# Performance work log

Hardware: AMD Instinct MI355X
Metric: run time of the kernel (lower is better)

The kernel has to match this reference:

```python
import jax, jax.numpy as jnp
import numpy as np
import math

EMBED = 768
HEADS = 12
DK = EMBED // HEADS
FFN = 3072
NQ = 8
B, S = 4, 2048


def _layernorm(x, g, b, eps=1e-5):
    mu = jnp.mean(x, axis=-1, keepdims=True)
    var = jnp.var(x, axis=-1, keepdims=True)
    return (x - mu) * jax.lax.rsqrt(var + eps) * g + b


def setup_inputs() -> dict:
    key = jax.random.key(0)
    ks = jax.random.split(key, 16)
    std = 0.02
    inp = {
        "x": jax.random.normal(ks[0], (B, S, EMBED), dtype=jnp.float32),
        "mask": jnp.ones((B, S), dtype=jnp.int32),
        # attention projections (torch Linear: W [out, in])
        "wq": jax.random.normal(ks[1], (EMBED, EMBED), jnp.float32) * std,
        "bq": jnp.zeros((EMBED,), jnp.float32),
        "wk": jax.random.normal(ks[2], (EMBED, EMBED), jnp.float32) * std,
        "bk": jnp.zeros((EMBED,), jnp.float32),
        "wv": jax.random.normal(ks[3], (EMBED, EMBED), jnp.float32) * std,
        "bv": jnp.zeros((EMBED,), jnp.float32),
        "wo": jax.random.normal(ks[4], (EMBED, EMBED), jnp.float32) * std,
        "bo": jnp.zeros((EMBED,), jnp.float32),
        # layernorms
        "g1": jnp.ones((EMBED,), jnp.float32),
        "be1": jnp.zeros((EMBED,), jnp.float32),
        "g2": jnp.ones((EMBED,), jnp.float32),
        "be2": jnp.zeros((EMBED,), jnp.float32),
        # quantum FFN: trainable RY angles + two linears
        "theta": jax.random.normal(ks[5], (NQ,), jnp.float32) * 0.1,
        "w1": jax.random.normal(ks[6], (FFN, NQ), jnp.float32) * std,
        "b1": jnp.zeros((FFN,), jnp.float32),
        "w2": jax.random.normal(ks[7], (EMBED, FFN), jnp.float32) * std,
        "b2": jnp.zeros((EMBED,), jnp.float32),
    }
    return inp


def _block(x, mask, wq, bq, wk, bk, wv, bv, wo, bo, g1, be1, g2, be2,
           theta, w1, b1, w2, b2):
    b, s, _ = x.shape
    # --- multi-head attention (dropout = identity at eval) ---
    q = (x @ wq.T + bq).reshape(b, s, HEADS, DK)
    k = (x @ wk.T + bk).reshape(b, s, HEADS, DK)
    v = (x @ wv.T + bv).reshape(b, s, HEADS, DK)
    scores = jnp.einsum("bqhd,bkhd->bhqk", q, k) / math.sqrt(DK)
    scores = jnp.where(mask[:, None, None, :] == 0, -1e9, scores)
    attn = jax.nn.softmax(scores, axis=-1)
    ctx = jnp.einsum("bhqk,bkhd->bqhd", attn, v).reshape(b, s, EMBED)
    attn_out = ctx @ wo.T + bo
    x = _layernorm(x + attn_out, g1, be1)
    # --- quantum FFN: RY(x_i) then RY(theta_i) on |0>, <Z> = cos(x_i+theta_i)
    # (product state, no entanglement -> exact closed form, fully batched)
    meas = jnp.cos(x[..., :NQ] + theta)            # [b, s, NQ]
    h = jax.nn.relu(meas @ w1.T + b1)              # [b, s, FFN]
    ffn_out = h @ w2.T + b2                        # [b, s, EMBED]
    return _layernorm(x + ffn_out, g2, be2)


def reference(x, mask, wq, bq, wk, bk, wv, bv, wo, bo, g1, be1, g2, be2,
              theta, w1, b1, w2, b2):
    return _block(x, mask, wq, bq, wk, bk, wv, bv, wo, bo,
                  g1, be1, g2, be2, theta, w1, b1, w2, b2)
```

## Files before the change

### kernel.cpp

```cpp
#include <hip/hip_runtime.h>
#include <hip/hip_bf16.h>


typedef __bf16 bf16_t;
typedef bf16_t bf16x4 __attribute__((ext_vector_type(4)));
typedef bf16_t bf16x8 __attribute__((ext_vector_type(8)));
typedef float floatx4 __attribute__((ext_vector_type(4)));

#define LOG2E 1.44269504088896f

__device__ __forceinline__ void gload16(const bf16_t* g, bf16_t* l) {
    __builtin_amdgcn_global_load_lds(
        (const __attribute__((address_space(1))) unsigned int*)g,
        (__attribute__((address_space(3))) unsigned int*)l,
        16, 0, 0);
}

__global__ __launch_bounds__(256)
void prep(const float* __restrict__ x,
          const float* __restrict__ wq, const float* __restrict__ wk,
          const float* __restrict__ wv, const float* __restrict__ wo,
          const float* __restrict__ w2, const float* __restrict__ w1,
          const float* __restrict__ bq, const float* __restrict__ bk,
          const float* __restrict__ bv,
          bf16_t* __restrict__ xb, bf16_t* __restrict__ wqkv,
          bf16_t* __restrict__ wob, bf16_t* __restrict__ w2b,
          bf16_t* __restrict__ w1b, float* __restrict__ bqkv)
{
    const int seg = blockIdx.y;
    const int idx = blockIdx.x * 256 + threadIdx.x;
    if (seg == 0) {
        if (idx >= 1572864) return;
        const float4 f = ((const float4*)x)[idx];
        bf16x4 o = {(bf16_t)f.x, (bf16_t)f.y, (bf16_t)f.z, (bf16_t)f.w};
        ((bf16x4*)xb)[idx] = o;
    } else if (seg == 1) {
        if (idx >= 442368) return;
        const int e = idx * 4;
        float4 f = (e < 589824) ? ((const float4*)wq)[idx]
                 : (e < 1179648) ? ((const float4*)wk)[idx - 147456]
                                 : ((const float4*)wv)[idx - 294912];
        if (e < 589824) { f.x *= 0.125f; f.y *= 0.125f; f.z *= 0.125f; f.w *= 0.125f; }
        bf16x4 o = {(bf16_t)f.x, (bf16_t)f.y, (bf16_t)f.z, (bf16_t)f.w};
        ((bf16x4*)wqkv)[idx] = o;
    } else if (seg == 2) {
        if (idx >= 147456) return;
        const float4 f = ((const float4*)wo)[idx];
        bf16x4 o = {(bf16_t)f.x, (bf16_t)f.y, (bf16_t)f.z, (bf16_t)f.w};
        ((bf16x4*)wob)[idx] = o;
    } else if (seg == 3) {
        if (idx >= 589824) return;
        const float4 f = ((const float4*)w2)[idx];
        bf16x4 o = {(bf16_t)f.x, (bf16_t)f.y, (bf16_t)f.z, (bf16_t)f.w};
        ((bf16x4*)w2b)[idx] = o;
    } else if (seg == 4) {
        if (idx >= 576) return;
        const int e = idx * 4;
        float4 f = (e < 768) ? ((const float4*)bq)[idx]
                 : (e < 1536) ? ((const float4*)bk)[idx - 192]
                              : ((const float4*)bv)[idx - 384];
        if (e < 768) { f.x *= 0.125f; f.y *= 0.125f; f.z *= 0.125f; f.w *= 0.125f; }
        ((float4*)bqkv)[idx] = f;
    } else {
        if (idx >= 6144) return;
        const float4 f = ((const float4*)w1)[idx];
        bf16x4 o = {(bf16_t)f.x, (bf16_t)f.y, (bf16_t)f.z, (bf16_t)f.w};
        ((bf16x4*)w1b)[idx] = o;
    }
}

template<typename TC>
__global__ __launch_bounds__(256)
void gemm_bb(const bf16_t* __restrict__ A, const bf16_t* __restrict__ W,
             const float* __restrict__ bias, TC* __restrict__ C,
             int kPer, int lda, int ldw, int ldc, int splitStride)
{
    __shared__ __align__(16) bf16_t As[2][4096];
    __shared__ __align__(16) bf16_t Bs[2][4096];
    const int tid  = threadIdx.x;
    const int wave = tid >> 6;
    const int lane = tid & 63;
    const int wm = (wave >> 1) * 64;
    const int wn = (wave & 1) * 64;

    const int nwg  = gridDim.x * gridDim.y;
    const int flat = blockIdx.y * gridDim.x + blockIdx.x;
    const int swzb = (flat & 7) * (nwg >> 3) + (flat >> 3);
    const int bm = (swzb / gridDim.x) * 128;
    const int bn = (swzb % gridDim.x) * 128;

    const int fr = lane & 15;
    const int fk = (lane >> 4) * 8;

    const int kBeg = blockIdx.z * kPer;
    const int kEnd = kBeg + kPer;
    C += (size_t)blockIdx.z * splitStride;

    const int srow = tid >> 2;
    const int scol = (tid & 3) * 8;

    floatx4 acc[4][4] = {};

    const bf16_t* gA = A + (size_t)(bm + srow) * lda + scol;
    const bf16_t* gB = W + (size_t)(bn + srow) * ldw + scol;

#define STAGE(buf, kk)                                              \
    {   const bf16_t* ga = gA + (kk);                               \
        const bf16_t* gb = gB + (kk);                               \
        gload16(ga,                    &As[buf][tid * 8]);          \
        gload16(ga + (size_t)64 * lda, &As[buf][tid * 8 + 2048]);   \
        gload16(gb,                    &Bs[buf][tid * 8]);          \
        gload16(gb + (size_t)64 * ldw, &Bs[buf][tid * 8 + 2048]);   \
    }

    STAGE(0, kBeg);
    __syncthreads();

    int cur = 0;
    for (int k0 = kBeg; k0 < kEnd; k0 += 32) {
        if (k0 + 32 < kEnd) STAGE(cur ^ 1, k0 + 32);

        bf16x8 fa[4], fb[4];
        #pragma unroll
        for (int i = 0; i < 4; ++i) {
            fa[i] = *(const bf16x8*)&As[cur][(wm + i * 16 + fr) * 32 + fk];
            fb[i] = *(const bf16x8*)&Bs[cur][(wn + i * 16 + fr) * 32 + fk];
        }
        #pragma unroll
        for (int mi = 0; mi < 4; ++mi)
            #pragma unroll
            for (int ni = 0; ni < 4; ++ni)
                acc[mi][ni] = __builtin_amdgcn_mfma_f32_16x16x32_bf16(
                    fa[mi], fb[ni], acc[mi][ni], 0, 0, 0);

        __syncthreads();
        cur ^= 1;
    }
#undef STAGE

    const int fg = (lane >> 4) * 4;
    const bool addb = (blockIdx.z == 0);
    #pragma unroll
    for (int mi = 0; mi < 4; ++mi) {
        #pragma unroll
        for (int ni = 0; ni < 4; ++ni) {
            const int col = bn + wn + ni * 16 + fr;
            const float bv = addb ? bias[col] : 0.f;
            #pragma unroll
            for (int r = 0; r < 4; ++r) {
                const int row = bm + wm + mi * 16 + fg + r;
                C[(size_t)row * ldc + col] = (TC)(acc[mi][ni][r] + bv);
            }
        }
    }
}

__global__ __launch_bounds__(256)
void attn_mfma(const bf16_t* __restrict__ qkv, const int* __restrict__ mask,
               bf16_t* __restrict__ ctx)
{
    __shared__ bf16_t Ks[64][72];
    __shared__ bf16_t Vt[80][72];
    __shared__ float  mb_s[64];
    __shared__ bf16_t Pl[4][32][72];

    const int flat = blockIdx.x;
    const int swzb = (flat & 7) * 96 + (flat >> 3);
    const int bh = swzb >> 4;
    const int b = bh / 12, h = bh % 12;
    const int tid  = threadIdx.x;
    const int wave = tid >> 6;
    const int lane = tid & 63;
    const int g    = lane >> 4;
    const int fr   = lane & 15;
    const int qbase = (swzb & 15) * 128 + wave * 32;

    for (int idx = tid; idx < 16 * 72; idx += 256) {
        const int rr = idx / 72, cc = idx % 72;
        Vt[64 + rr][cc] = (bf16_t)(rr == 0 ? 1.f : 0.f);
    }

    bf16x8 qf[2][2];
    #pragma unroll
    for (int qt = 0; qt < 2; ++qt)
        #pragma unroll
        for (int s = 0; s < 2; ++s) {
            const size_t tok = (size_t)(b * 2048 + qbase + qt * 16 + fr);
            qf[qt][s] = *(const bf16x8*)(qkv + tok * 2304 + h * 64 + s * 32 + g * 8);
        }

    floatx4 o[2][4] = {};
    floatx4 oe[2] = {};

    const int skey = tid & 63;
    const int sgrp = tid >> 6;

    bf16x8 rk0, rk1, rv0, rv1;
    float  rmb;
    {
        const size_t ktok = (size_t)(b * 2048 + skey) * 2304 + h * 64;
        rk0 = *(const bf16x8*)(qkv + ktok + 768 + sgrp * 16);
        rk1 = *(const bf16x8*)(qkv + ktok + 768 + sgrp * 16 + 8);
        rv0 = *(const bf16x8*)(qkv + ktok + 1536 + sgrp * 16);
        rv1 = *(const bf16x8*)(qkv + ktok + 1536 + sgrp * 16 + 8);
        rmb = (mask[b * 2048 + skey] == 0) ? -1e9f : 0.f;
    }

    for (int kt = 0; kt < 32; ++kt) {
        __syncthreads();
        *(bf16x8*)&Ks[skey][sgrp * 16]     = rk0;
        *(bf16x8*)&Ks[skey][sgrp * 16 + 8] = rk1;
        #pragma unroll
        for (int j = 0; j < 8; ++j) {
            Vt[sgrp * 16 + j][skey]     = rv0[j];
            Vt[sgrp * 16 + 8 + j][skey] = rv1[j];
        }
        if (tid < 64) mb_s[tid] = rmb;
        __syncthreads();

        if (kt + 1 < 32) {
            const size_t ktok = (size_t)(b * 2048 + (kt + 1) * 64 + skey) * 2304 + h * 64;
            rk0 = *(const bf16x8*)(qkv + ktok + 768 + sgrp * 16);
            rk1 = *(const bf16x8*)(qkv + ktok + 768 + sgrp * 16 + 8);
            rv0 = *(const bf16x8*)(qkv + ktok + 1536 + sgrp * 16);
            rv1 = *(const bf16x8*)(qkv + ktok + 1536 + sgrp * 16 + 8);
            rmb = (mask[b * 2048 + (kt + 1) * 64 + skey] == 0) ? -1e9f : 0.f;
        }

        floatx4 st_[2][4] = {};
        #pragma unroll
        for (int s = 0; s < 2; ++s) {
            bf16x8 kf[4];
            #pragma unroll
            for (int ct = 0; ct < 4; ++ct)
                kf[ct] = *(const bf16x8*)&Ks[ct * 16 + fr][s * 32 + g * 8];
            #pragma unroll
            for (int qt = 0; qt < 2; ++qt)
                #pragma unroll
                for (int ct = 0; ct < 4; ++ct)
                    st_[qt][ct] = __builtin_amdgcn_mfma_f32_16x16x32_bf16(
                        kf[ct], qf[qt][s], st_[qt][ct], 0, 0, 0);
        }

        #pragma unroll
        for (int qt = 0; qt < 2; ++qt) {
            #pragma unroll
            for (int ct = 0; ct < 4; ++ct) {
                const float4 mb4 = *(const float4*)&mb_s[ct * 16 + g * 4];
                const float mbr[4] = { mb4.x, mb4.y, mb4.z, mb4.w };
                bf16x4 pw;
                #pragma unroll
                for (int r = 0; r < 4; ++r)
                    pw[r] = (bf16_t)__builtin_amdgcn_exp2f(
                        fmaf(st_[qt][ct][r], LOG2E, mbr[r]));
                *(bf16x4*)&Pl[wave][qt * 16 + fr][ct * 16 + g * 4] = pw;
            }
        }

        #pragma unroll
        for (int st2 = 0; st2 < 2; ++st2) {
            bf16x8 pf[2];
            #pragma unroll
            for (int qt = 0; qt < 2; ++qt)
                pf[qt] = *(const bf16x8*)&Pl[wave][qt * 16 + fr][st2 * 32 + g * 8];
            #pragma unroll
            for (int dt = 0; dt < 4; ++dt) {
                const bf16x8 vf = *(const bf16x8*)&Vt[dt * 16 + fr][st2 * 32 + g * 8];
                #pragma unroll
                for (int qt = 0; qt < 2; ++qt)
                    o[qt][dt] = __builtin_amdgcn_mfma_f32_16x16x32_bf16(
                        pf[qt], vf, o[qt][dt], 0, 0, 0);
            }
            const bf16x8 vo = *(const bf16x8*)&Vt[64 + fr][st2 * 32 + g * 8];
            #pragma unroll
            for (int qt = 0; qt < 2; ++qt)
                oe[qt] = __builtin_amdgcn_mfma_f32_16x16x32_bf16(
                    pf[qt], vo, oe[qt], 0, 0, 0);
        }
    }

    #pragma unroll
    for (int qt = 0; qt < 2; ++qt) {
        float inv[4];
        #pragma unroll
        for (int r = 0; r < 4; ++r) {
            const float lv = __shfl(oe[qt][r], (lane & 48), 64);
            inv[r] = 1.f / lv;
        }
        #pragma unroll
        for (int dt = 0; dt < 4; ++dt)
            #pragma unroll
            for (int r = 0; r < 4; ++r) {
                const size_t row = (size_t)(b * 2048 + qbase + qt * 16 + g * 4 + r);
                ctx[row * 768 + h * 64 + dt * 16 + fr] = (bf16_t)(o[qt][dt][r] * inv[r]);
            }
    }
}

__global__ __launch_bounds__(256)
void ln_fuse(const float* __restrict__ xin, const float* __restrict__ proj,
             const float* __restrict__ proj2,
             const float* __restrict__ g, const float* __restrict__ be,
             float* __restrict__ out,
             const float* __restrict__ theta, float* __restrict__ meas)
{
    const int wave = threadIdx.x >> 6;
    const int lane = threadIdx.x & 63;
    const int row  = blockIdx.x * 4 + wave;
    const size_t base = (size_t)row * 768;

    float4 v[3];
    float s1 = 0.f, s2 = 0.f;
    #pragma unroll
    for (int i = 0; i < 3; ++i) {
        const int c4 = lane + i * 64;
        const float4 a  = ((const float4*)(xin  + base))[c4];
        const float4 p  = ((const float4*)(proj + base))[c4];
        const float4 p2 = ((const float4*)(proj2 + base))[c4];
        v[i].x = a.x + p.x + p2.x;
        v[i].y = a.y + p.y + p2.y;
        v[i].z = a.z + p.z + p2.z;
        v[i].w = a.w + p.w + p2.w;
        s1 += v[i].x + v[i].y + v[i].z + v[i].w;
        s2 += v[i].x*v[i].x + v[i].y*v[i].y + v[i].z*v[i].z + v[i].w*v[i].w;
    }
    #pragma unroll
    for (int mk = 32; mk >= 1; mk >>= 1) {
        s1 += __shfl_xor(s1, mk, 64);
        s2 += __shfl_xor(s2, mk, 64);
    }
    const float mu   = s1 * (1.f / 768.f);
    const float var  = s2 * (1.f / 768.f) - mu * mu;
    const float rinv = rsqrtf(var + 1e-5f);

    #pragma unroll
    for (int i = 0; i < 3; ++i) {
        const int c4 = lane + i * 64;
        const float4 gg = ((const float4*)g)[c4];
        const float4 bb = ((const float4*)be)[c4];
        float4 o;
        o.x = (v[i].x - mu) * rinv * gg.x + bb.x;
        o.y = (v[i].y - mu) * rinv * gg.y + bb.y;
        o.z = (v[i].z - mu) * rinv * gg.z + bb.z;
        o.w = (v[i].w - mu) * rinv * gg.w + bb.w;
        ((float4*)(out + base))[c4] = o;
        if (i == 0 && meas != nullptr && lane < 2) {
            meas[row * 8 + lane * 4 + 0] = cosf(o.x + theta[lane * 4 + 0]);
            meas[row * 8 + lane * 4 + 1] = cosf(o.y + theta[lane * 4 + 1]);
            meas[row * 8 + lane * 4 + 2] = cosf(o.z + theta[lane * 4 + 2]);
            meas[row * 8 + lane * 4 + 3] = cosf(o.w + theta[lane * 4 + 3]);
        }
    }
}

__global__ __launch_bounds__(256)
void ffn1(const float* __restrict__ meas, const bf16_t* __restrict__ w1b,
          const float* __restrict__ b1, bf16_t* __restrict__ h)
{
    const int row0 = blockIdx.x * 4;
    __shared__ float ms[4][8];
    if (threadIdx.x < 32)
        ms[threadIdx.x >> 3][threadIdx.x & 7] = meas[row0 * 8 + threadIdx.x];
    __syncthreads();
    #pragma unroll
    for (int i = 0; i < 12; ++i) {
        const int f = threadIdx.x + i * 256;
        const bf16x8 w = *(const bf16x8*)(w1b + f * 8);
        float wv[8];
        #pragma unroll
        for (int j = 0; j < 8; ++j) wv[j] = (float)w[j];
        const float bias = b1[f];
        #pragma unroll
        for (int r = 0; r < 4; ++r) {
            float v = bias;
            #pragma unroll
            for (int j = 0; j < 8; ++j) v += ms[r][j] * wv[j];
            h[(size_t)(row0 + r) * 3072 + f] = (bf16_t)fmaxf(v, 0.f);
        }
    }
}

extern "C" void kernel_launch(void* const* d_in, const int* in_sizes, int n_in,
                              void* d_out, int out_size, void* d_ws, size_t ws_size,
                              hipStream_t stream)
{
    const float* x     = (const float*)d_in[0];
    const int*   mask  = (const int*)d_in[1];
    const float* wq    = (const float*)d_in[2];
    const float* bq    = (const float*)d_in[3];
    const float* wk    = (const float*)d_in[4];
    const float* bk    = (const float*)d_in[5];
    const float* wv    = (const float*)d_in[6];
    const float* bv    = (const float*)d_in[7];
    const float* wo    = (const float*)d_in[8];
    const float* bo    = (const float*)d_in[9];
    const float* g1    = (const float*)d_in[10];
    const float* be1   = (const float*)d_in[11];
    const float* g2    = (const float*)d_in[12];
    const float* be2   = (const float*)d_in[13];
    const float* theta = (const float*)d_in[14];
    const float* w1    = (const float*)d_in[15];
    const float* b1    = (const float*)d_in[16];
    const float* w2    = (const float*)d_in[17];
    const float* b2    = (const float*)d_in[18];
    float* out = (float*)d_out;

    char* ws = (char*)d_ws;
    bf16_t* qkv    = (bf16_t*)(ws + 0);
    bf16_t* ctx    = (bf16_t*)(ws + 37748736);
    float*  attnp  = (float*)(ws + 50331648);
    float*  y      = (float*)(ws + 100663296);
    float*  meas   = (float*)(ws + 125829120);
    bf16_t* xb     = (bf16_t*)(ws + 126091264);
    bf16_t* wqkv   = (bf16_t*)(ws + 138674176);
    bf16_t* wob    = (bf16_t*)(ws + 142213120);
    bf16_t* w2b    = (bf16_t*)(ws + 143392768);
    float*  bqkv   = (float*)(ws + 148111360);
    bf16_t* w1b    = (bf16_t*)(ws + 148120576);
    float*  ffnp   = (float*)(ws + 0);
    bf16_t* h      = (bf16_t*)(ws + 50331648);

    const dim3 blk(256);

    prep<<<dim3(6144, 6), blk, 0, stream>>>(x, wq, wk, wv, wo, w2, w1, bq, bk, bv,
                                            xb, wqkv, wob, w2b, w1b, bqkv);

    gemm_bb<bf16_t><<<dim3(18, 64, 1), blk, 0, stream>>>(
        xb, wqkv, bqkv, qkv, 768, 768, 768, 2304, 0);

    attn_mfma<<<dim3(768), blk, 0, stream>>>(qkv, mask, ctx);

    gemm_bb<float><<<dim3(6, 64, 2), blk, 0, stream>>>(
        ctx, wob, bo, attnp, 384, 768, 768, 768, 6291456);

    ln_fuse<<<dim3(2048), blk, 0, stream>>>(x, attnp, attnp + 6291456,
                                            g1, be1, y, theta, meas);

    ffn1<<<dim3(2048), blk, 0, stream>>>(meas, w1b, b1, h);

    gemm_bb<float><<<dim3(6, 64, 2), blk, 0, stream>>>(
        h, w2b, b2, ffnp, 1536, 3072, 3072, 768, 6291456);

    ln_fuse<<<dim3(2048), blk, 0, stream>>>(y, ffnp, ffnp + 6291456,
                                            g2, be2, out, nullptr, nullptr);
}
```

Measured before the change: 279.1 us.

## Emit head-major swizzled K/V from QKV GEMM and stream K via direct LDS loads

Adds a dedicated QKV GEMM whose epilogue writes Q token-major and K and V in a per-(batch, head) contiguous layout, with K columns XOR-swizzled by row. The attention kernel then streams each 64-key K tile straight into double-buffered LDS with global_load_lds, and loads V as contiguous 16-byte chunks instead of strided per-token reads. The aim is to remove register staging and bank conflicts for K and to make K/V fetches coalesced. In exchange the GEMM epilogue does scattered 2-byte stores into the head-major layout, and LDS use grows because K is now double-buffered.

```diff
diff --git a/kernel.cpp b/kernel.cpp
--- a/kernel.cpp
+++ b/kernel.cpp
@@ -156,10 +156,107 @@
 }
 
 __global__ __launch_bounds__(256)
-void attn_mfma(const bf16_t* __restrict__ qkv, const int* __restrict__ mask,
+void gemm_qkv(const bf16_t* __restrict__ A, const bf16_t* __restrict__ W0,
+              const float* __restrict__ bias0,
+              bf16_t* __restrict__ Qb, bf16_t* __restrict__ Kh,
+              bf16_t* __restrict__ Vh)
+{
+    __shared__ __align__(16) bf16_t As[2][4096];
+    __shared__ __align__(16) bf16_t Bs[2][4096];
+    const int tid  = threadIdx.x;
+    const int wave = tid >> 6;
+    const int lane = tid & 63;
+    const int wm = (wave >> 1) * 64;
+    const int wn = (wave & 1) * 64;
+
+    const int nwg  = gridDim.x * gridDim.y;
+    const int flat = blockIdx.y * gridDim.x + blockIdx.x;
+    const int swzb = (flat & 7) * (nwg >> 3) + (flat >> 3);
+    const int tx = swzb % gridDim.x;
+    const int bm = (swzb / gridDim.x) * 128;
+    const int sect = tx / 6;
+    const int bn = (tx % 6) * 128;
+    const bf16_t* W    = W0 + (size_t)sect * 589824;
+    const float* bias  = bias0 + sect * 768;
+
+    const int fr = lane & 15;
+    const int fk = (lane >> 4) * 8;
+    const int srow = tid >> 2;
+    const int scol = (tid & 3) * 8;
+
+    floatx4 acc[4][4] = {};
+
+    const bf16_t* gA = A + (size_t)(bm + srow) * 768 + scol;
+    const bf16_t* gB = W + (size_t)(bn + srow) * 768 + scol;
+
+#define STAGEQ(buf, kk)                                             \
+    {   const bf16_t* ga = gA + (kk);                               \
+        const bf16_t* gb = gB + (kk);                               \
+        gload16(ga,                   &As[buf][tid * 8]);           \
+        gload16(ga + (size_t)64*768,  &As[buf][tid * 8 + 2048]);    \
+        gload16(gb,                   &Bs[buf][tid * 8]);           \
+        gload16(gb + (size_t)64*768,  &Bs[buf][tid * 8 + 2048]);    \
+    }
+
+    STAGEQ(0, 0);
+    __syncthreads();
+
+    int cur = 0;
+    for (int k0 = 0; k0 < 768; k0 += 32) {
+        if (k0 + 32 < 768) STAGEQ(cur ^ 1, k0 + 32);
+
+        bf16x8 fa[4], fb[4];
+        #pragma unroll
+        for (int i = 0; i < 4; ++i) {
+            fa[i] = *(const bf16x8*)&As[cur][(wm + i * 16 + fr) * 32 + fk];
+            fb[i] = *(const bf16x8*)&Bs[cur][(wn + i * 16 + fr) * 32 + fk];
+        }
+        #pragma unroll
+        for (int mi = 0; mi < 4; ++mi)
+            #pragma unroll
+            for (int ni = 0; ni < 4; ++ni)
+                acc[mi][ni] = __builtin_amdgcn_mfma_f32_16x16x32_bf16(
+                    fa[mi], fb[ni], acc[mi][ni], 0, 0, 0);
+
+        __syncthreads();
+        cur ^= 1;
+    }
+#undef STAGEQ
+
+    const int fg = (lane >> 4) * 4;
+    #pragma unroll
+    for (int mi = 0; mi < 4; ++mi) {
+        #pragma unroll
+        for (int ni = 0; ni < 4; ++ni) {
+            const int col = bn + wn + ni * 16 + fr;
+            const float bv = bias[col];
+            #pragma unroll
+            for (int r = 0; r < 4; ++r) {
+                const int row = bm + wm + mi * 16 + fg + r;
+                const bf16_t val = (bf16_t)(acc[mi][ni][r] + bv);
+                if (sect == 0) {
+                    Qb[(size_t)row * 768 + col] = val;
+                } else {
+                    const int head = col >> 6;
+                    const int d    = col & 63;
+                    const size_t base =
+                        ((size_t)((row >> 11) * 12 + head) * 2048 + (row & 2047)) * 64;
+                    if (sect == 1)
+                        Kh[base + (d ^ ((row & 7) << 3))] = val;
+                    else
+                        Vh[base + d] = val;
+                }
+            }
+        }
+    }
+}
+
+__global__ __launch_bounds__(256)
+void attn_mfma(const bf16_t* __restrict__ Qb, const bf16_t* __restrict__ Kh,
+               const bf16_t* __restrict__ Vh, const int* __restrict__ mask,
                bf16_t* __restrict__ ctx)
 {
-    __shared__ bf16_t Ks[64][72];
+    __shared__ __align__(16) bf16_t KsL[2][4096];
     __shared__ bf16_t Vt[80][72];
     __shared__ float  mb_s[64];
     __shared__ bf16_t Pl[4][32][72];
@@ -186,45 +283,41 @@
         #pragma unroll
         for (int s = 0; s < 2; ++s) {
             const size_t tok = (size_t)(b * 2048 + qbase + qt * 16 + fr);
-            qf[qt][s] = *(const bf16x8*)(qkv + tok * 2304 + h * 64 + s * 32 + g * 8);
+            qf[qt][s] = *(const bf16x8*)(Qb + tok * 768 + h * 64 + s * 32 + g * 8);
         }
 
     floatx4 o[2][4] = {};
     floatx4 oe[2] = {};
 
-    const int skey = tid & 63;
-    const int sgrp = tid >> 6;
-
-    bf16x8 rk0, rk1, rv0, rv1;
-    float  rmb;
-    {
-        const size_t ktok = (size_t)(b * 2048 + skey) * 2304 + h * 64;
-        rk0 = *(const bf16x8*)(qkv + ktok + 768 + sgrp * 16);
-        rk1 = *(const bf16x8*)(qkv + ktok + 768 + sgrp * 16 + 8);
-        rv0 = *(const bf16x8*)(qkv + ktok + 1536 + sgrp * 16);
-        rv1 = *(const bf16x8*)(qkv + ktok + 1536 + sgrp * 16 + 8);
-        rmb = (mask[b * 2048 + skey] == 0) ? -1e9f : 0.f;
-    }
-
+    const bf16_t* kbase = Kh + (size_t)bh * 131072;
+    const bf16_t* vbase = Vh + (size_t)bh * 131072;
+    const int c0 = tid, c1 = tid + 256;
+
+    gload16(kbase + c0 * 8, &KsL[0][c0 * 8]);
+    gload16(kbase + c0 * 8 + 2048, &KsL[0][c0 * 8 + 2048]);
+    bf16x8 rv0 = *(const bf16x8*)(vbase + c0 * 8);
+    bf16x8 rv1 = *(const bf16x8*)(vbase + c1 * 8);
+    float  rmb = (mask[b * 2048 + (tid & 63)] == 0) ? -1e9f : 0.f;
+
+    int cur = 0;
     for (int kt = 0; kt < 32; ++kt) {
         __syncthreads();
-        *(bf16x8*)&Ks[skey][sgrp * 16]     = rk0;
-        *(bf16x8*)&Ks[skey][sgrp * 16 + 8] = rk1;
         #pragma unroll
         for (int j = 0; j < 8; ++j) {
-            Vt[sgrp * 16 + j][skey]     = rv0[j];
-            Vt[sgrp * 16 + 8 + j][skey] = rv1[j];
+            Vt[(c0 & 7) * 8 + j][c0 >> 3] = rv0[j];
+            Vt[(c1 & 7) * 8 + j][c1 >> 3] = rv1[j];
         }
         if (tid < 64) mb_s[tid] = rmb;
         __syncthreads();
 
         if (kt + 1 < 32) {
-            const size_t ktok = (size_t)(b * 2048 + (kt + 1) * 64 + skey) * 2304 + h * 64;
-            rk0 = *(const bf16x8*)(qkv + ktok + 768 + sgrp * 16);
-            rk1 = *(const bf16x8*)(qkv + ktok + 768 + sgrp * 16 + 8);
-            rv0 = *(const bf16x8*)(qkv + ktok + 1536 + sgrp * 16);
-            rv1 = *(const bf16x8*)(qkv + ktok + 1536 + sgrp * 16 + 8);
-            rmb = (mask[b * 2048 + (kt + 1) * 64 + skey] == 0) ? -1e9f : 0.f;
+            const bf16_t* knext = kbase + (kt + 1) * 4096;
+            gload16(knext + c0 * 8, &KsL[cur ^ 1][c0 * 8]);
+            gload16(knext + c0 * 8 + 2048, &KsL[cur ^ 1][c0 * 8 + 2048]);
+            const bf16_t* vnext = vbase + (kt + 1) * 4096;
+            rv0 = *(const bf16x8*)(vnext + c0 * 8);
+            rv1 = *(const bf16x8*)(vnext + c1 * 8);
+            rmb = (mask[b * 2048 + (kt + 1) * 64 + (tid & 63)] == 0) ? -1e9f : 0.f;
         }
 
         floatx4 st_[2][4] = {};
@@ -232,8 +325,11 @@
         for (int s = 0; s < 2; ++s) {
             bf16x8 kf[4];
             #pragma unroll
-            for (int ct = 0; ct < 4; ++ct)
-                kf[ct] = *(const bf16x8*)&Ks[ct * 16 + fr][s * 32 + g * 8];
+            for (int ct = 0; ct < 4; ++ct) {
+                const int krow = ct * 16 + fr;
+                const int kcol = (s * 32 + g * 8) ^ ((krow & 7) << 3);
+                kf[ct] = *(const bf16x8*)&KsL[cur][krow * 64 + kcol];
+            }
             #pragma unroll
             for (int qt = 0; qt < 2; ++qt)
                 #pragma unroll
@@ -277,6 +373,8 @@
                 oe[qt] = __builtin_amdgcn_mfma_f32_16x16x32_bf16(
                     pf[qt], vo, oe[qt], 0, 0, 0);
         }
+
+        cur ^= 1;
     }
 
     #pragma unroll
@@ -406,7 +504,9 @@
     float* out = (float*)d_out;
 
     char* ws = (char*)d_ws;
-    bf16_t* qkv    = (bf16_t*)(ws + 0);
+    bf16_t* Qb     = (bf16_t*)(ws + 0);
+    bf16_t* Kh     = (bf16_t*)(ws + 12582912);
+    bf16_t* Vh     = (bf16_t*)(ws + 25165824);
     bf16_t* ctx    = (bf16_t*)(ws + 37748736);
     float*  attnp  = (float*)(ws + 50331648);
     float*  y      = (float*)(ws + 100663296);
@@ -425,10 +525,9 @@
     prep<<<dim3(6144, 6), blk, 0, stream>>>(x, wq, wk, wv, wo, w2, w1, bq, bk, bv,
                                             xb, wqkv, wob, w2b, w1b, bqkv);
 
-    gemm_bb<bf16_t><<<dim3(18, 64, 1), blk, 0, stream>>>(
-        xb, wqkv, bqkv, qkv, 768, 768, 768, 2304, 0);
-
-    attn_mfma<<<dim3(768), blk, 0, stream>>>(qkv, mask, ctx);
+    gemm_qkv<<<dim3(18, 64), blk, 0, stream>>>(xb, wqkv, bqkv, Qb, Kh, Vh);
+
+    attn_mfma<<<dim3(768), blk, 0, stream>>>(Qb, Kh, Vh, mask, ctx);
 
     gemm_bb<float><<<dim3(6, 64, 2), blk, 0, stream>>>(
         ctx, wob, bo, attnp, 384, 768, 768, 768, 6291456);
```

Measured after the change: 305.3 us. 9.4% more time.

## Split attention key range in two and add a combine kernel

Applied to the files above, without the earlier changes.

Each attention block now processes only half of the key tiles, which doubles the grid to 1536 blocks. Each block writes unnormalized fp32 partial outputs and row sums to workspace. A new attn_combine kernel adds the two halves, normalizes them and writes the bf16 context. The goal is more parallelism and better CU load balance, at the cost of extra fp32 partial traffic through global memory and one more kernel launch.

```diff
diff --git a/kernel.cpp b/kernel.cpp
--- a/kernel.cpp
+++ b/kernel.cpp
@@ -157,7 +157,7 @@
 
 __global__ __launch_bounds__(256)
 void attn_mfma(const bf16_t* __restrict__ qkv, const int* __restrict__ mask,
-               bf16_t* __restrict__ ctx)
+               float* __restrict__ op, float* __restrict__ lp)
 {
     __shared__ bf16_t Ks[64][72];
     __shared__ bf16_t Vt[80][72];
@@ -165,15 +165,19 @@
     __shared__ bf16_t Pl[4][32][72];
 
     const int flat = blockIdx.x;
-    const int swzb = (flat & 7) * 96 + (flat >> 3);
-    const int bh = swzb >> 4;
+    const int swz  = (flat & 7) * 192 + (flat >> 3);
+    const int bh   = swz >> 5;
+    const int rem  = swz & 31;
+    const int qidx = rem >> 1;
+    const int half = rem & 1;
     const int b = bh / 12, h = bh % 12;
     const int tid  = threadIdx.x;
     const int wave = tid >> 6;
     const int lane = tid & 63;
     const int g    = lane >> 4;
     const int fr   = lane & 15;
-    const int qbase = (swzb & 15) * 128 + wave * 32;
+    const int qbase = qidx * 128 + wave * 32;
+    const int ktBeg = half * 16, ktEnd = ktBeg + 16;
 
     for (int idx = tid; idx < 16 * 72; idx += 256) {
         const int rr = idx / 72, cc = idx % 72;
@@ -198,15 +202,15 @@
     bf16x8 rk0, rk1, rv0, rv1;
     float  rmb;
     {
-        const size_t ktok = (size_t)(b * 2048 + skey) * 2304 + h * 64;
+        const size_t ktok = (size_t)(b * 2048 + ktBeg * 64 + skey) * 2304 + h * 64;
         rk0 = *(const bf16x8*)(qkv + ktok + 768 + sgrp * 16);
         rk1 = *(const bf16x8*)(qkv + ktok + 768 + sgrp * 16 + 8);
         rv0 = *(const bf16x8*)(qkv + ktok + 1536 + sgrp * 16);
         rv1 = *(const bf16x8*)(qkv + ktok + 1536 + sgrp * 16 + 8);
-        rmb = (mask[b * 2048 + skey] == 0) ? -1e9f : 0.f;
-    }
-
-    for (int kt = 0; kt < 32; ++kt) {
+        rmb = (mask[b * 2048 + ktBeg * 64 + skey] == 0) ? -1e9f : 0.f;
+    }
+
+    for (int kt = ktBeg; kt < ktEnd; ++kt) {
         __syncthreads();
         *(bf16x8*)&Ks[skey][sgrp * 16]     = rk0;
         *(bf16x8*)&Ks[skey][sgrp * 16 + 8] = rk1;
@@ -218,7 +222,7 @@
         if (tid < 64) mb_s[tid] = rmb;
         __syncthreads();
 
-        if (kt + 1 < 32) {
+        if (kt + 1 < ktEnd) {
             const size_t ktok = (size_t)(b * 2048 + (kt + 1) * 64 + skey) * 2304 + h * 64;
             rk0 = *(const bf16x8*)(qkv + ktok + 768 + sgrp * 16);
             rk1 = *(const bf16x8*)(qkv + ktok + 768 + sgrp * 16 + 8);
@@ -279,21 +283,48 @@
         }
     }
 
+    float* opH = op + (size_t)half * 6291456;
     #pragma unroll
     for (int qt = 0; qt < 2; ++qt) {
-        float inv[4];
-        #pragma unroll
-        for (int r = 0; r < 4; ++r) {
-            const float lv = __shfl(oe[qt][r], (lane & 48), 64);
-            inv[r] = 1.f / lv;
-        }
         #pragma unroll
         for (int dt = 0; dt < 4; ++dt)
             #pragma unroll
             for (int r = 0; r < 4; ++r) {
                 const size_t row = (size_t)(b * 2048 + qbase + qt * 16 + g * 4 + r);
-                ctx[row * 768 + h * 64 + dt * 16 + fr] = (bf16_t)(o[qt][dt][r] * inv[r]);
+                opH[row * 768 + h * 64 + dt * 16 + fr] = o[qt][dt][r];
             }
+        if (fr == 0) {
+            #pragma unroll
+            for (int r = 0; r < 4; ++r) {
+                const size_t row = (size_t)(b * 2048 + qbase + qt * 16 + g * 4 + r);
+                lp[(size_t)half * 98304 + row * 12 + h] = oe[qt][r];
+            }
+        }
+    }
+}
+
+__global__ __launch_bounds__(256)
+void attn_combine(const float* __restrict__ op, const float* __restrict__ lp,
+                  bf16_t* __restrict__ ctx)
+{
+    const int wave = threadIdx.x >> 6;
+    const int lane = threadIdx.x & 63;
+    const int row  = blockIdx.x * 4 + wave;
+    const size_t base = (size_t)row * 768;
+    #pragma unroll
+    for (int i = 0; i < 3; ++i) {
+        const int c4 = lane + i * 64;
+        const int head = c4 >> 4;
+        const float inv = 1.f / (lp[(size_t)row * 12 + head] +
+                                 lp[98304 + (size_t)row * 12 + head]);
+        const float4 a = ((const float4*)(op + base))[c4];
+        const float4 c = ((const float4*)(op + 6291456 + base))[c4];
+        bf16x4 o4;
+        o4[0] = (bf16_t)((a.x + c.x) * inv);
+        o4[1] = (bf16_t)((a.y + c.y) * inv);
+        o4[2] = (bf16_t)((a.z + c.z) * inv);
+        o4[3] = (bf16_t)((a.w + c.w) * inv);
+        ((bf16x4*)(ctx + base))[c4] = o4;
     }
 }
 
@@ -409,9 +440,11 @@
     bf16_t* qkv    = (bf16_t*)(ws + 0);
     bf16_t* ctx    = (bf16_t*)(ws + 37748736);
     float*  attnp  = (float*)(ws + 50331648);
+    float*  opart  = (float*)(ws + 50331648);
     float*  y      = (float*)(ws + 100663296);
     float*  meas   = (float*)(ws + 125829120);
     bf16_t* xb     = (bf16_t*)(ws + 126091264);
+    float*  lpart  = (float*)(ws + 126091264);
     bf16_t* wqkv   = (bf16_t*)(ws + 138674176);
     bf16_t* wob    = (bf16_t*)(ws + 142213120);
     bf16_t* w2b    = (bf16_t*)(ws + 143392768);
@@ -428,7 +461,8 @@
     gemm_bb<bf16_t><<<dim3(18, 64, 1), blk, 0, stream>>>(
         xb, wqkv, bqkv, qkv, 768, 768, 768, 2304, 0);
 
-    attn_mfma<<<dim3(768), blk, 0, stream>>>(qkv, mask, ctx);
+    attn_mfma<<<dim3(1536), blk, 0, stream>>>(qkv, mask, opart, lpart);
+    attn_combine<<<dim3(2048), blk, 0, stream>>>(opart, lpart, ctx);
 
     gemm_bb<float><<<dim3(6, 64, 2), blk, 0, stream>>>(
         ctx, wob, bo, attnp, 384, 768, 768, 768, 6291456);
```

After: 292.9 us. 1.05x slower.
